# Performance work log

Measured on AMD Instinct MI355X. Metric: run time of the kernel, lower is better.

Reference implementation:

```python
import jax, jax.numpy as jnp
import numpy as np

D_MODEL, D_K, D_V, H = 1024, 64, 64, 16
B, NQ, NK = 4, 1024, 1024


def setup_inputs() -> dict:
    key = jax.random.key(0)
    ks = jax.random.split(key, 16)
    xav = lambda k, shape: jax.random.uniform(k, shape, jnp.float32, -1.0, 1.0) * np.sqrt(6.0 / (shape[0] + shape[1])).astype(np.float32)
    return {
        "queries": jax.random.normal(ks[0], (B, NQ, D_MODEL), jnp.float32),
        "keys": jax.random.normal(ks[1], (B, NK, D_MODEL), jnp.float32),
        "values": jax.random.normal(ks[2], (B, NK, D_MODEL), jnp.float32),
        "attention_weights": jax.random.uniform(ks[3], (B, H, NQ, NK), jnp.float32),
        "attention_mask": jax.random.randint(ks[4], (B, H, NQ, NK), 0, 2, jnp.int32),
        "Wq": xav(ks[5], (H * D_K, D_MODEL)), "bq": jnp.zeros((H * D_K,), jnp.float32),
        "Wk": xav(ks[6], (H * D_K, D_MODEL)), "bk": jnp.zeros((H * D_K,), jnp.float32),
        "Wv": xav(ks[7], (H * D_V, D_MODEL)), "bv": jnp.zeros((H * D_V,), jnp.float32),
        "Wo": xav(ks[8], (D_MODEL, H * D_V)), "bo": jnp.zeros((D_MODEL,), jnp.float32),
    }


def reference(queries, keys, values, attention_weights, attention_mask,
              Wq, bq, Wk, bk, Wv, bv, Wo, bo):
    b, nq, _ = queries.shape
    nk = keys.shape[1]
    # projections, split heads: (b, h, n, d)
    q = (queries @ Wq.T + bq).reshape(b, nq, H, D_K).transpose(0, 2, 1, 3)
    k = (keys @ Wk.T + bk).reshape(b, nk, H, D_K).transpose(0, 2, 1, 3)
    v = (values @ Wv.T + bv).reshape(b, nk, H, D_V).transpose(0, 2, 1, 3)
    scale = jnp.asarray(1.0 / np.sqrt(D_K), q.dtype)
    att = jnp.einsum('bhqd,bhkd->bhqk', q, k) * scale
    att_map = att  # returned pre-bias/mask scores, as in the torch code (att.clone())
    # way='mul', use_knn=False path
    att = att * attention_weights
    att = jnp.where(attention_mask == 0, -jnp.inf, att)
    att = jax.nn.softmax(att, axis=-1)
    out = jnp.einsum('bhqk,bhkd->bqhd', att, v).reshape(b, nq, H * D_V)
    out = out @ Wo.T + bo
    return out, att_map
```

## Files before the change

kernel.cpp:

```cpp
#include <hip/hip_runtime.h>
#include <stdint.h>
#include <math.h>

#define B_ 4
#define H_ 16
#define DM_ 1024
#define NQ_ 1024
#define NK_ 1024

typedef __attribute__((ext_vector_type(4))) float f32x4;
typedef __attribute__((ext_vector_type(4))) int   s32x4;
typedef __attribute__((ext_vector_type(4))) short s16x4;
typedef __attribute__((ext_vector_type(8))) short s16x8;

#define MFMA(a, b, c) __builtin_amdgcn_mfma_f32_16x16x32_bf16(a, b, c, 0, 0, 0)

static __device__ __forceinline__ short f2bf(float f) {
  union { float f; uint32_t u; } v; v.f = f;
  uint32_t r = (v.u + 0x7FFFu + ((v.u >> 16) & 1u)) >> 16;
  return (short)(uint16_t)r;
}

static __device__ __forceinline__ float bf2f(short s) {
  union { uint32_t u; float f; } v;
  v.u = ((uint32_t)(uint16_t)s) << 16;
  return v.f;
}

static __device__ __forceinline__ void gload_lds16(const void* g, void* s) {
  __builtin_amdgcn_global_load_lds(
      (const __attribute__((address_space(1))) uint32_t*)g,
      (__attribute__((address_space(3))) uint32_t*)s, 16, 0, 0);
}

__global__ void k_cvt(const float* __restrict__ src, short* __restrict__ dst, int n) {
  int i = (blockIdx.x * 256 + threadIdx.x) * 4;
  if (i + 3 < n) {
    f32x4 v = *(const f32x4*)(src + i);
    s16x4 o;
    o.x = f2bf(v.x); o.y = f2bf(v.y); o.z = f2bf(v.z); o.w = f2bf(v.w);
    *(s16x4*)(dst + i) = o;
  }
}

__global__ __launch_bounds__(256, 2) void k_gemm(
    const short* __restrict__ A, const short* __restrict__ Bw,
    const float* __restrict__ bias, void* __restrict__ outp, int mode) {
  __shared__ short As[128 * 64];
  __shared__ short Bs[128 * 64];
  const int tid = threadIdx.x;
  const int w = tid >> 6, l = tid & 63;
  const int wm = w >> 1, wn = w & 1;
  const int lr = l & 15, lg = l >> 4;
  const int m0 = blockIdx.x * 128, n0 = blockIdx.y * 128;

  f32x4 acc[4][4] = {};

  for (int kt = 0; kt < 16; ++kt) {
    __syncthreads();
#pragma unroll
    for (int q = 0; q < 4; ++q) {
      const int slot = (w * 4 + q) * 64 + l;
      const int row = slot >> 3;
      const int chunk = (slot & 7) ^ (row & 7);
      const size_t goff = (size_t)row * 1024 + (size_t)kt * 64 + chunk * 8;
      gload_lds16(A + (size_t)m0 * 1024 + goff, (char*)As + (w * 4 + q) * 1024);
      gload_lds16(Bw + (size_t)n0 * 1024 + goff, (char*)Bs + (w * 4 + q) * 1024);
    }
    asm volatile("s_waitcnt vmcnt(0)");
    __syncthreads();
#pragma unroll
    for (int ks = 0; ks < 2; ++ks) {
      s16x8 af[4], bfr[4];
#pragma unroll
      for (int mi = 0; mi < 4; ++mi) {
        const int row = wm * 64 + mi * 16 + lr;
        const int chunk = (ks * 4 + lg) ^ (row & 7);
        af[mi] = *(const s16x8*)(As + row * 64 + chunk * 8);
      }
#pragma unroll
      for (int ni = 0; ni < 4; ++ni) {
        const int row = wn * 64 + ni * 16 + lr;
        const int chunk = (ks * 4 + lg) ^ (row & 7);
        bfr[ni] = *(const s16x8*)(Bs + row * 64 + chunk * 8);
      }
#pragma unroll
      for (int mi = 0; mi < 4; ++mi)
#pragma unroll
        for (int ni = 0; ni < 4; ++ni)
          acc[mi][ni] = MFMA(af[mi], bfr[ni], acc[mi][ni]);
    }
  }

#pragma unroll
  for (int mi = 0; mi < 4; ++mi) {
#pragma unroll
    for (int ni = 0; ni < 4; ++ni) {
      const int gm0 = m0 + wm * 64 + mi * 16 + lg * 4;
      const int gc = n0 + wn * 64 + ni * 16 + lr;
      const float bv = bias[gc];
      if (mode == 2) {
        float* o = (float*)outp;
#pragma unroll
        for (int r = 0; r < 4; ++r)
          o[(size_t)(gm0 + r) * 1024 + gc] = acc[mi][ni][r] + bv;
      } else if (mode == 0) {
        short* o = (short*)outp;
        const int h = gc >> 6, d = gc & 63;
#pragma unroll
        for (int r = 0; r < 4; ++r) {
          const int gm = gm0 + r;
          const int b = gm >> 10, np = gm & 1023;
          o[((size_t)(b * 16 + h) * 1024 + np) * 64 + d] = f2bf(acc[mi][ni][r] + bv);
        }
      } else {
        short* o = (short*)outp;
        const int h = gc >> 6, d = gc & 63;
        const int b = gm0 >> 10, np0 = gm0 & 1023;
        s16x4 pk;
        pk.x = f2bf(acc[mi][ni][0] + bv);
        pk.y = f2bf(acc[mi][ni][1] + bv);
        pk.z = f2bf(acc[mi][ni][2] + bv);
        pk.w = f2bf(acc[mi][ni][3] + bv);
        *(s16x4*)(o + ((size_t)(b * 16 + h) * 64 + d) * 1024 + np0) = pk;
      }
    }
  }
}

__global__ __launch_bounds__(256, 3) void k_attn(
    const short* __restrict__ qws, const short* __restrict__ kws,
    const short* __restrict__ vtws,
    const float* __restrict__ attw, const int* __restrict__ attm,
    float* __restrict__ att_map, short* __restrict__ o_part,
    float* __restrict__ mpart, float* __restrict__ lpart) {
  __shared__ f32x4 s_lds[4 * 256];
  __shared__ short p_lds[4 * 16 * 64];
  __shared__ float st_lds[4 * 16];
  const int tid = threadIdx.x;
  const int w = tid >> 6, l = tid & 63;
  const int lr = l & 15, lg = l >> 4;
  const int bh = blockIdx.y;
  const int split = blockIdx.z;
  const int q0 = blockIdx.x * 64 + w * 16;
  f32x4* const sw = s_lds + w * 256;
  char* const pw = (char*)p_lds + w * 2048;
  float* const stw = st_lds + w * 16;

  const short* qb = qws + ((size_t)bh * NQ_ + q0 + lr) * 64 + lg * 8;
  const s16x8 qf0 = *(const s16x8*)(qb);
  const s16x8 qf1 = *(const s16x8*)(qb + 32);

  f32x4 o[4] = {};
  float m4[4], l4[4];
#pragma unroll
  for (int it = 0; it < 4; ++it) { m4[it] = -3.0e38f; l4[it] = 0.0f; }

  const size_t linBase = ((size_t)bh * NQ_ + q0 + lg) * (size_t)NK_ + lr * 4;

  for (int kt = split * 8; kt < split * 8 + 8; ++kt) {
    f32x4 s[4];
    const short* kb0 = kws + ((size_t)bh * NK_ + kt * 64 + lr) * 64 + lg * 8;
#pragma unroll
    for (int fn = 0; fn < 4; ++fn) {
      const short* kb = kb0 + fn * 1024;
      f32x4 z = {};
      z = MFMA(*(const s16x8*)kb, qf0, z);
      z = MFMA(*(const s16x8*)(kb + 32), qf1, z);
      s[fn] = z;
    }
#pragma unroll
    for (int fn = 0; fn < 4; ++fn)
      sw[lr * 16 + ((fn * 4 + lg) ^ lr)] = s[fn];
    asm volatile("s_waitcnt lgkmcnt(0)" ::: "memory");
    __builtin_amdgcn_sched_barrier(0);
    f32x4 sv4[4], wv4[4];
    s32x4 mv4[4];
#pragma unroll
    for (int it = 0; it < 4; ++it) {
      const int q = it * 4 + lg;
      sv4[it] = sw[q * 16 + (lr ^ q)];
      const size_t ga = linBase + (size_t)(it * 4) * NK_ + kt * 64;
      wv4[it] = *(const f32x4*)(attw + ga);
      mv4[it] = *(const s32x4*)(attm + ga);
    }
#pragma unroll
    for (int it = 0; it < 4; ++it) {
      const int q = it * 4 + lg;
      f32x4 sv;
#pragma unroll
      for (int j = 0; j < 4; ++j) sv[j] = sv4[it][j] * 0.125f;
      const size_t ga = linBase + (size_t)(it * 4) * NK_ + kt * 64;
      *(f32x4*)(att_map + ga) = sv;
      float p[4];
#pragma unroll
      for (int j = 0; j < 4; ++j)
        p[j] = mv4[it][j] ? sv[j] * wv4[it][j] : -1.0e30f;
      float t = fmaxf(fmaxf(p[0], p[1]), fmaxf(p[2], p[3]));
      t = fmaxf(t, __shfl_xor(t, 1, 64));
      t = fmaxf(t, __shfl_xor(t, 2, 64));
      t = fmaxf(t, __shfl_xor(t, 4, 64));
      t = fmaxf(t, __shfl_xor(t, 8, 64));
      const float mn = fmaxf(m4[it], t);
      const float corr = __expf(m4[it] - mn);
      m4[it] = mn;
      float rs = 0.0f;
#pragma unroll
      for (int j = 0; j < 4; ++j) { p[j] = __expf(p[j] - mn); rs += p[j]; }
      rs += __shfl_xor(rs, 1, 64);
      rs += __shfl_xor(rs, 2, 64);
      rs += __shfl_xor(rs, 4, 64);
      rs += __shfl_xor(rs, 8, 64);
      l4[it] = l4[it] * corr + rs;
      s16x4 pk;
      pk.x = f2bf(p[0]); pk.y = f2bf(p[1]); pk.z = f2bf(p[2]); pk.w = f2bf(p[3]);
      *(s16x4*)(pw + q * 128 + (((lr >> 1) ^ (q & 7)) << 4) + (lr & 1) * 8) = pk;
      if (lr == 0) stw[q] = corr;
    }
    asm volatile("s_waitcnt lgkmcnt(0)" ::: "memory");
    __builtin_amdgcn_sched_barrier(0);
#pragma unroll
    for (int r = 0; r < 4; ++r) {
      const float cr = stw[lg * 4 + r];
      o[0][r] *= cr; o[1][r] *= cr; o[2][r] *= cr; o[3][r] *= cr;
    }
    const short* vb0 = vtws + ((size_t)bh * 64 + lr) * (size_t)NK_ + (size_t)kt * 64 + lg * 8;
#pragma unroll
    for (int ks = 0; ks < 2; ++ks) {
      const int chunk = (ks * 4 + lg) ^ (lr & 7);
      const s16x8 pa = *(const s16x8*)(pw + lr * 128 + chunk * 16);
#pragma unroll
      for (int g = 0; g < 4; ++g) {
        const s16x8 vf = *(const s16x8*)(vb0 + (size_t)g * 16 * NK_ + ks * 32);
        o[g] = MFMA(pa, vf, o[g]);
      }
    }
  }

  short* op = o_part + (size_t)split * 4194304;
  const int qrow_base = bh * NQ_ + q0 + lg * 4;
#pragma unroll
  for (int r = 0; r < 4; ++r) {
    const size_t orow = (size_t)(qrow_base + r) * 64 + lr;
#pragma unroll
    for (int g = 0; g < 4; ++g)
      op[orow + g * 16] = f2bf(o[g][r]);
  }
  if (lr == 0) {
#pragma unroll
    for (int it = 0; it < 4; ++it) {
      const int qrow = bh * NQ_ + q0 + it * 4 + lg;
      mpart[split * 65536 + qrow] = m4[it];
      lpart[split * 65536 + qrow] = l4[it];
    }
  }
}

__global__ __launch_bounds__(256, 4) void k_merge(
    const short* __restrict__ o_part, const float* __restrict__ mpart,
    const float* __restrict__ lpart, short* __restrict__ aout) {
  const int t = blockIdx.x * 256 + threadIdx.x;
  const int row = t >> 4;
  const int d0 = (t & 15) * 4;
  const float m1 = mpart[row], m2 = mpart[65536 + row];
  const float l1 = lpart[row], l2 = lpart[65536 + row];
  const float M = fmaxf(m1, m2);
  const float c1 = __expf(m1 - M), c2 = __expf(m2 - M);
  const float inv = 1.0f / (l1 * c1 + l2 * c2);
  const s16x4 a = *(const s16x4*)(o_part + (size_t)row * 64 + d0);
  const s16x4 b = *(const s16x4*)(o_part + 4194304 + (size_t)row * 64 + d0);
  const int bh = row >> 10, q = row & 1023;
  const int bb = bh >> 4, h = bh & 15;
  s16x4 o;
#pragma unroll
  for (int j = 0; j < 4; ++j)
    o[j] = f2bf((bf2f(a[j]) * c1 + bf2f(b[j]) * c2) * inv);
  *(s16x4*)(aout + ((size_t)(bb * 1024 + q) * 1024 + h * 64 + d0)) = o;
}

extern "C" void kernel_launch(void* const* d_in, const int* in_sizes, int n_in,
                              void* d_out, int out_size, void* d_ws, size_t ws_size,
                              hipStream_t stream) {
  const float* queries = (const float*)d_in[0];
  const float* keys    = (const float*)d_in[1];
  const float* values  = (const float*)d_in[2];
  const float* attw    = (const float*)d_in[3];
  const int*   attm    = (const int*)d_in[4];
  const float* Wq = (const float*)d_in[5];
  const float* bq = (const float*)d_in[6];
  const float* Wk = (const float*)d_in[7];
  const float* bk = (const float*)d_in[8];
  const float* Wv = (const float*)d_in[9];
  const float* bv = (const float*)d_in[10];
  const float* Wo = (const float*)d_in[11];
  const float* bo = (const float*)d_in[12];

  float* out = (float*)d_out;
  float* att_map = out + (size_t)B_ * NQ_ * DM_;

  short* ws  = (short*)d_ws;
  short* WqB = ws;
  short* WkB = WqB + 1048576;
  short* WvB = WkB + 1048576;
  short* WoB = WvB + 1048576;
  short* Xq  = WoB + 1048576;
  short* Xk  = Xq + 4194304;
  short* Xv  = Xk + 4194304;
  short* qws = Xv + 4194304;
  short* kws = qws + 4194304;
  short* vtw = kws + 4194304;
  short* aout = vtw + 4194304;

  short* o_part = Xq;
  float* mpart  = (float*)Xv;
  float* lpart  = mpart + 131072;

  k_cvt<<<4096, 256, 0, stream>>>(queries, Xq, 4194304);
  k_cvt<<<4096, 256, 0, stream>>>(keys, Xk, 4194304);
  k_cvt<<<4096, 256, 0, stream>>>(values, Xv, 4194304);
  k_cvt<<<1024, 256, 0, stream>>>(Wq, WqB, 1048576);
  k_cvt<<<1024, 256, 0, stream>>>(Wk, WkB, 1048576);
  k_cvt<<<1024, 256, 0, stream>>>(Wv, WvB, 1048576);
  k_cvt<<<1024, 256, 0, stream>>>(Wo, WoB, 1048576);

  dim3 gg(32, 8);
  k_gemm<<<gg, 256, 0, stream>>>(Xq, WqB, bq, qws, 0);
  k_gemm<<<gg, 256, 0, stream>>>(Xk, WkB, bk, kws, 0);
  k_gemm<<<gg, 256, 0, stream>>>(Xv, WvB, bv, vtw, 1);

  dim3 ga(16, 64, 2);
  k_attn<<<ga, 256, 0, stream>>>(qws, kws, vtw, attw, attm, att_map,
                                 o_part, mpart, lpart);
  k_merge<<<4096, 256, 0, stream>>>(o_part, mpart, lpart, aout);

  k_gemm<<<gg, 256, 0, stream>>>(aout, WoB, bo, out, 2);
}
```

Measured before the change: 377.1 us.

## Stage full 512-key score rows in LDS and run a two-pass row softmax

The attention kernel now has three phases. It first computes all QK scores for its 512-key split and stores them as bf16 in LDS. It then walks each query row with fully contiguous 2KB loads of the weights and mask, computes an exact max and sum per row, and writes the probabilities back into LDS. Finally it runs the PV MFMAs over that buffer. This removes the per-tile online-softmax rescaling and the scattered 16-byte global accesses, at the cost of 64KB of LDS per block (occupancy bound lowered to 2). The att_map output is now written from bf16-rounded scores instead of fp32, which loses precision.

```diff
diff --git a/kernel.cpp b/kernel.cpp
--- a/kernel.cpp
+++ b/kernel.cpp
@@ -128,107 +128,105 @@
   }
 }
 
-__global__ __launch_bounds__(256, 3) void k_attn(
+__global__ __launch_bounds__(256, 2) void k_attn(
     const short* __restrict__ qws, const short* __restrict__ kws,
     const short* __restrict__ vtws,
     const float* __restrict__ attw, const int* __restrict__ attm,
     float* __restrict__ att_map, short* __restrict__ o_part,
     float* __restrict__ mpart, float* __restrict__ lpart) {
-  __shared__ f32x4 s_lds[4 * 256];
-  __shared__ short p_lds[4 * 16 * 64];
-  __shared__ float st_lds[4 * 16];
+  __shared__ short s_lds[4 * 16 * 512];
   const int tid = threadIdx.x;
-  const int w = tid >> 6, l = tid & 63;
-  const int lr = l & 15, lg = l >> 4;
+  const int w = tid >> 6, ln = tid & 63;
+  const int lr = ln & 15, lg = ln >> 4;
   const int bh = blockIdx.y;
   const int split = blockIdx.z;
   const int q0 = blockIdx.x * 64 + w * 16;
-  f32x4* const sw = s_lds + w * 256;
-  char* const pw = (char*)p_lds + w * 2048;
-  float* const stw = st_lds + w * 16;
+  short* const sw = s_lds + w * (16 * 512);
+  const int k0 = split * 512;
 
   const short* qb = qws + ((size_t)bh * NQ_ + q0 + lr) * 64 + lg * 8;
   const s16x8 qf0 = *(const s16x8*)(qb);
   const s16x8 qf1 = *(const s16x8*)(qb + 32);
 
-  f32x4 o[4] = {};
-  float m4[4], l4[4];
-#pragma unroll
-  for (int it = 0; it < 4; ++it) { m4[it] = -3.0e38f; l4[it] = 0.0f; }
-
-  const size_t linBase = ((size_t)bh * NQ_ + q0 + lg) * (size_t)NK_ + lr * 4;
-
-  for (int kt = split * 8; kt < split * 8 + 8; ++kt) {
-    f32x4 s[4];
-    const short* kb0 = kws + ((size_t)bh * NK_ + kt * 64 + lr) * 64 + lg * 8;
+  for (int st = 0; st < 8; ++st) {
+    const short* kb0 = kws + ((size_t)bh * NK_ + k0 + st * 64 + lr) * 64 + lg * 8;
 #pragma unroll
     for (int fn = 0; fn < 4; ++fn) {
       const short* kb = kb0 + fn * 1024;
       f32x4 z = {};
       z = MFMA(*(const s16x8*)kb, qf0, z);
       z = MFMA(*(const s16x8*)(kb + 32), qf1, z);
-      s[fn] = z;
-    }
-#pragma unroll
-    for (int fn = 0; fn < 4; ++fn)
-      sw[lr * 16 + ((fn * 4 + lg) ^ lr)] = s[fn];
-    asm volatile("s_waitcnt lgkmcnt(0)" ::: "memory");
-    __builtin_amdgcn_sched_barrier(0);
-    f32x4 sv4[4], wv4[4];
-    s32x4 mv4[4];
-#pragma unroll
-    for (int it = 0; it < 4; ++it) {
-      const int q = it * 4 + lg;
-      sv4[it] = sw[q * 16 + (lr ^ q)];
-      const size_t ga = linBase + (size_t)(it * 4) * NK_ + kt * 64;
-      wv4[it] = *(const f32x4*)(attw + ga);
-      mv4[it] = *(const s32x4*)(attm + ga);
-    }
-#pragma unroll
-    for (int it = 0; it < 4; ++it) {
-      const int q = it * 4 + lg;
-      f32x4 sv;
-#pragma unroll
-      for (int j = 0; j < 4; ++j) sv[j] = sv4[it][j] * 0.125f;
-      const size_t ga = linBase + (size_t)(it * 4) * NK_ + kt * 64;
-      *(f32x4*)(att_map + ga) = sv;
-      float p[4];
-#pragma unroll
-      for (int j = 0; j < 4; ++j)
-        p[j] = mv4[it][j] ? sv[j] * wv4[it][j] : -1.0e30f;
-      float t = fmaxf(fmaxf(p[0], p[1]), fmaxf(p[2], p[3]));
-      t = fmaxf(t, __shfl_xor(t, 1, 64));
-      t = fmaxf(t, __shfl_xor(t, 2, 64));
-      t = fmaxf(t, __shfl_xor(t, 4, 64));
-      t = fmaxf(t, __shfl_xor(t, 8, 64));
-      const float mn = fmaxf(m4[it], t);
-      const float corr = __expf(m4[it] - mn);
-      m4[it] = mn;
-      float rs = 0.0f;
-#pragma unroll
-      for (int j = 0; j < 4; ++j) { p[j] = __expf(p[j] - mn); rs += p[j]; }
-      rs += __shfl_xor(rs, 1, 64);
-      rs += __shfl_xor(rs, 2, 64);
-      rs += __shfl_xor(rs, 4, 64);
-      rs += __shfl_xor(rs, 8, 64);
-      l4[it] = l4[it] * corr + rs;
       s16x4 pk;
-      pk.x = f2bf(p[0]); pk.y = f2bf(p[1]); pk.z = f2bf(p[2]); pk.w = f2bf(p[3]);
-      *(s16x4*)(pw + q * 128 + (((lr >> 1) ^ (q & 7)) << 4) + (lr & 1) * 8) = pk;
-      if (lr == 0) stw[q] = corr;
-    }
-    asm volatile("s_waitcnt lgkmcnt(0)" ::: "memory");
-    __builtin_amdgcn_sched_barrier(0);
-#pragma unroll
-    for (int r = 0; r < 4; ++r) {
-      const float cr = stw[lg * 4 + r];
-      o[0][r] *= cr; o[1][r] *= cr; o[2][r] *= cr; o[3][r] *= cr;
-    }
-    const short* vb0 = vtws + ((size_t)bh * 64 + lr) * (size_t)NK_ + (size_t)kt * 64 + lg * 8;
+      pk.x = f2bf(z[0] * 0.125f); pk.y = f2bf(z[1] * 0.125f);
+      pk.z = f2bf(z[2] * 0.125f); pk.w = f2bf(z[3] * 0.125f);
+      const int c = st * 8 + fn * 2 + (lg >> 1);
+      *(s16x4*)((char*)sw + lr * 1024 + ((c ^ lr) << 4) + (lg & 1) * 8) = pk;
+    }
+  }
+  asm volatile("s_waitcnt lgkmcnt(0)" ::: "memory");
+  __builtin_amdgcn_sched_barrier(0);
+
+  const int rot = (blockIdx.x + bh + w) & 15;
+  float m16 = -3.0e38f, l16 = 0.0f;
+#pragma unroll 4
+  for (int j = 0; j < 16; ++j) {
+    const int jj = (j + rot) & 15;
+    const size_t rowb = ((size_t)bh * NQ_ + q0 + jj) * (size_t)NK_ + k0;
+    const f32x4 wv0 = *(const f32x4*)(attw + rowb + ln * 4);
+    const f32x4 wv1 = *(const f32x4*)(attw + rowb + 256 + ln * 4);
+    const s32x4 mv0 = *(const s32x4*)(attm + rowb + ln * 4);
+    const s32x4 mv1 = *(const s32x4*)(attm + rowb + 256 + ln * 4);
+    char* const rbase = (char*)sw + jj * 1024 + (ln & 1) * 8;
+    const int c0 = (((ln >> 1)) ^ jj) << 4;
+    const int c1 = ((32 + (ln >> 1)) ^ jj) << 4;
+    const s16x4 s0 = *(const s16x4*)(rbase + c0);
+    const s16x4 s1 = *(const s16x4*)(rbase + c1);
+    f32x4 a0, a1;
+#pragma unroll
+    for (int i = 0; i < 4; ++i) { a0[i] = bf2f(s0[i]); a1[i] = bf2f(s1[i]); }
+    *(f32x4*)(att_map + rowb + ln * 4) = a0;
+    *(f32x4*)(att_map + rowb + 256 + ln * 4) = a1;
+    float x0[4], x1[4];
+#pragma unroll
+    for (int i = 0; i < 4; ++i) {
+      x0[i] = mv0[i] ? a0[i] * wv0[i] : -1.0e30f;
+      x1[i] = mv1[i] ? a1[i] * wv1[i] : -1.0e30f;
+    }
+    float t = fmaxf(fmaxf(fmaxf(x0[0], x0[1]), fmaxf(x0[2], x0[3])),
+                    fmaxf(fmaxf(x1[0], x1[1]), fmaxf(x1[2], x1[3])));
+    t = fmaxf(t, __shfl_xor(t, 1, 64));
+    t = fmaxf(t, __shfl_xor(t, 2, 64));
+    t = fmaxf(t, __shfl_xor(t, 4, 64));
+    t = fmaxf(t, __shfl_xor(t, 8, 64));
+    t = fmaxf(t, __shfl_xor(t, 16, 64));
+    t = fmaxf(t, __shfl_xor(t, 32, 64));
+    float rs = 0.0f;
+    s16x4 p0, p1;
+#pragma unroll
+    for (int i = 0; i < 4; ++i) {
+      const float e0 = __expf(x0[i] - t); rs += e0; p0[i] = f2bf(e0);
+      const float e1 = __expf(x1[i] - t); rs += e1; p1[i] = f2bf(e1);
+    }
+    rs += __shfl_xor(rs, 1, 64);
+    rs += __shfl_xor(rs, 2, 64);
+    rs += __shfl_xor(rs, 4, 64);
+    rs += __shfl_xor(rs, 8, 64);
+    rs += __shfl_xor(rs, 16, 64);
+    rs += __shfl_xor(rs, 32, 64);
+    if (ln == jj) { m16 = t; l16 = rs; }
+    *(s16x4*)(rbase + c0) = p0;
+    *(s16x4*)(rbase + c1) = p1;
+  }
+  asm volatile("s_waitcnt lgkmcnt(0)" ::: "memory");
+  __builtin_amdgcn_sched_barrier(0);
+
+  f32x4 o[4] = {};
+  for (int st = 0; st < 8; ++st) {
+    const short* vb0 = vtws + ((size_t)bh * 64 + lr) * (size_t)NK_ + k0 + st * 64 + lg * 8;
 #pragma unroll
     for (int ks = 0; ks < 2; ++ks) {
-      const int chunk = (ks * 4 + lg) ^ (lr & 7);
-      const s16x8 pa = *(const s16x8*)(pw + lr * 128 + chunk * 16);
+      const int c = (st * 8 + ks * 4 + lg) ^ lr;
+      const s16x8 pa = *(const s16x8*)((char*)sw + lr * 1024 + (c << 4));
 #pragma unroll
       for (int g = 0; g < 4; ++g) {
         const s16x8 vf = *(const s16x8*)(vb0 + (size_t)g * 16 * NK_ + ks * 32);
@@ -246,13 +244,9 @@
     for (int g = 0; g < 4; ++g)
       op[orow + g * 16] = f2bf(o[g][r]);
   }
-  if (lr == 0) {
-#pragma unroll
-    for (int it = 0; it < 4; ++it) {
-      const int qrow = bh * NQ_ + q0 + it * 4 + lg;
-      mpart[split * 65536 + qrow] = m4[it];
-      lpart[split * 65536 + qrow] = l4[it];
-    }
+  if (ln < 16) {
+    mpart[split * 65536 + bh * NQ_ + q0 + ln] = m16;
+    lpart[split * 65536 + bh * NQ_ + q0 + ln] = l16;
   }
 }
 
```

New measurement: 368.9 us. 2.2% less time.
